# Optimization experiments

Hardware: AMD Instinct MI355X
Metric: run time of the kernel (lower is better)

## Reference

```python
import jax, jax.numpy as jnp
import numpy as np

N = 100000   # nodes
E = 1000000  # directed edges
IN = 32      # atom feature dim
H = 64       # hidden_channels
ED = 16      # edge_dim
OUT = 1      # out_channels
G = 512      # graphs in batch
SLOPE = 0.2  # GATConv leaky_relu negative_slope


def setup_inputs() -> dict:
    key = jax.random.key(0)
    ks = jax.random.split(key, 20)
    s = 0.1
    return {
        'x': jax.random.normal(ks[0], (N, IN), dtype=jnp.float32),
        'edge_attr': jax.random.normal(ks[1], (E, ED), dtype=jnp.float32),
        'w_node': jax.random.normal(ks[2], (IN, H), dtype=jnp.float32) * s,
        'b_node': jnp.zeros((H,), jnp.float32),
        'w_edge': jax.random.normal(ks[3], (ED, H), dtype=jnp.float32) * s,
        'b_edge': jnp.zeros((H,), jnp.float32),
        'conv_W': jax.random.normal(ks[4], (3, H, H), dtype=jnp.float32) * s,
        'conv_We': jax.random.normal(ks[5], (3, H, H), dtype=jnp.float32) * s,
        'conv_att_s': jax.random.normal(ks[6], (3, H), dtype=jnp.float32) * s,
        'conv_att_d': jax.random.normal(ks[7], (3, H), dtype=jnp.float32) * s,
        'conv_att_e': jax.random.normal(ks[8], (3, H), dtype=jnp.float32) * s,
        'conv_b': jnp.zeros((3, H), jnp.float32),
        'gru_Wih': jax.random.normal(ks[9], (3, H, 3 * H), dtype=jnp.float32) * s,
        'gru_Whh': jax.random.normal(ks[10], (3, H, 3 * H), dtype=jnp.float32) * s,
        'gru_bih': jnp.zeros((3, 3 * H), jnp.float32),
        'gru_bhh': jnp.zeros((3, 3 * H), jnp.float32),
        'w_out': jax.random.normal(ks[11], (H, OUT), dtype=jnp.float32) * s,
        'b_out': jnp.zeros((OUT,), jnp.float32),
        'edge_index': jax.random.randint(ks[12], (2, E), 0, N),
        'batch': jnp.sort(jax.random.randint(ks[13], (N,), 0, G)),
    }


def _gat_layer(x, e, src, dst, W, att_s, att_d, att_e, b):
    # PyG GATConv (heads=1, concat=False): shared lin for src/dst,
    # edge features enter only the attention score.
    h = x @ W                                   # [N, H]
    a = jax.nn.leaky_relu(h[src] @ att_s + h[dst] @ att_d + e @ att_e, SLOPE)
    m = jax.lax.stop_gradient(jax.ops.segment_max(a, dst, num_segments=N))
    m = jnp.where(jnp.isfinite(m), m, 0.0)
    ex = jnp.exp(a - m[dst])
    den = jax.ops.segment_sum(ex, dst, num_segments=N)
    alpha = ex / den[dst]                       # segment softmax per destination
    out = jax.ops.segment_sum(alpha[:, None] * h[src], dst, num_segments=N)
    return out + b


def _gru_cell(inp, hid, Wih, Whh, bih, bhh):
    gi = inp @ Wih + bih
    gh = hid @ Whh + bhh
    ir, iz, inn = jnp.split(gi, 3, axis=-1)
    hr, hz, hn = jnp.split(gh, 3, axis=-1)
    r = jax.nn.sigmoid(ir + hr)
    z = jax.nn.sigmoid(iz + hz)
    n = jnp.tanh(inn + r * hn)
    return (1.0 - z) * n + z * hid


def reference(x, edge_attr, w_node, b_node, w_edge, b_edge, conv_W, conv_We,
              conv_att_s, conv_att_d, conv_att_e, conv_b, gru_Wih, gru_Whh,
              gru_bih, gru_bhh, w_out, b_out, edge_index, batch):
    src, dst = edge_index[0], edge_index[1]
    xi = jax.nn.relu(x @ w_node + b_node)             # [N, H]
    ea = jax.nn.relu(edge_attr @ w_edge + b_edge)     # [E, H]
    # PyG add_self_loops(fill_value='mean'): self-loop edge_attr = mean of
    # incoming edge_attr per destination node (0 if no in-edges).
    cnt = jax.ops.segment_sum(jnp.ones((E,), xi.dtype), dst, num_segments=N)
    esum = jax.ops.segment_sum(ea, dst, num_segments=N)
    ea_loop = jnp.where(cnt[:, None] > 0, esum / jnp.maximum(cnt, 1.0)[:, None], 0.0)
    loops = jnp.arange(N)
    src2 = jnp.concatenate([src, loops])
    dst2 = jnp.concatenate([dst, loops])
    ea2 = jnp.concatenate([ea, ea_loop], axis=0)      # [E+N, H]
    for i in range(3):
        e = ea2 @ conv_We[i]
        h = jax.nn.relu(_gat_layer(xi, e, src2, dst2, conv_W[i],
                                   conv_att_s[i], conv_att_d[i],
                                   conv_att_e[i], conv_b[i]))
        # dropout p=0.0 is identity
        xi = jax.nn.relu(_gru_cell(h, xi, gru_Wih[i], gru_Whh[i],
                                   gru_bih[i], gru_bhh[i]))
    pooled = jax.ops.segment_sum(xi, batch, num_segments=G)  # global_add_pool
    return pooled @ w_out + b_out                            # [G, 1]
```

## Files before the change

### kernel.cpp

```cpp
#include <hip/hip_runtime.h>
#include <hip/hip_fp16.h>

constexpr int H_  = 64;
constexpr int DIN = 32;
constexpr int DE  = 16;
constexpr int BNODE = 512;
constexpr int ACH   = 2048;
constexpr int CAP   = 6144;
#define SLOPE 0.2f

typedef __attribute__((ext_vector_type(8))) short bf16x8;
typedef __attribute__((ext_vector_type(4))) float f32x4;

__device__ __forceinline__ float sigm_(float x){ return 1.0f/(1.0f+__expf(-x)); }
__device__ __forceinline__ float tanh_(float x){ float e=__expf(2.0f*x); return 1.0f - 2.0f/(e+1.0f); }
__device__ __forceinline__ short f2bf(float f){
  unsigned u = __float_as_uint(f);
  u += 0x7FFF + ((u>>16)&1);
  return (short)(u>>16);
}
__device__ __forceinline__ float bf2f(unsigned short s){
  return __uint_as_float(((unsigned)s)<<16);
}
__device__ __forceinline__ float h2f_(unsigned hb){
  return __half2float(__ushort_as_half((unsigned short)hb));
}

__global__ void k_prep(const float* __restrict__ w_node, const float* __restrict__ w_edge,
                       const float* __restrict__ conv_W, const float* __restrict__ gWih,
                       const float* __restrict__ gWhh, const float* __restrict__ conv_We,
                       const float* __restrict__ att_e,
                       short* __restrict__ wnT16, short* __restrict__ weT16p,
                       short* __restrict__ cWT16, short* __restrict__ WihT16,
                       short* __restrict__ WhhT16, float* __restrict__ ve,
                       int* __restrict__ bcur){
  int id = blockIdx.x*blockDim.x + threadIdx.x;
  if (id < 2048){
    int j = id >> 5, k = id & 31;
    wnT16[id] = f2bf(w_node[k*64 + j]);
    return;
  }
  id -= 2048;
  if (id < 2048){
    int j = id >> 5, k = id & 31;
    weT16p[id] = (k < DE) ? f2bf(w_edge[k*64 + j]) : (short)0;
    return;
  }
  id -= 2048;
  if (id < 12288){
    int l = id / 4096, rem = id & 4095, j = rem >> 6, k = rem & 63;
    cWT16[id] = f2bf(conv_W[l*4096 + k*64 + j]);
    return;
  }
  id -= 12288;
  if (id < 36864){
    int l = id / 12288, rem = id % 12288, j = rem >> 6, k = rem & 63;
    WihT16[id] = f2bf(gWih[l*12288 + k*192 + j]);
    return;
  }
  id -= 36864;
  if (id < 36864){
    int l = id / 12288, rem = id % 12288, j = rem >> 6, k = rem & 63;
    WhhT16[id] = f2bf(gWhh[l*12288 + k*192 + j]);
    return;
  }
  id -= 36864;
  if (id < 192){
    int l = id >> 6, k = id & 63;
    const float* w = conv_We + (size_t)(l*64+k)*64;
    const float* a = att_e + l*64;
    float s = 0.f;
    #pragma unroll
    for (int j=0;j<64;j++) s += w[j]*a[j];
    ve[id] = s;
    return;
  }
  id -= 192;
  if (id < 256) bcur[id] = id*CAP;
}

__global__ void __launch_bounds__(256,4)
k_nmlp_m(const float* __restrict__ x, const short* __restrict__ wT16,
         const float* __restrict__ b, short* __restrict__ xi, int N){
  int lane = threadIdx.x & 63, w = threadIdx.x >> 6;
  int m16 = lane & 15, kb = lane >> 4;
  int n0 = blockIdx.x*64 + w*16;
  int arow = n0 + m16; if (arow > N-1) arow = N-1;
  const float* xr = x + (size_t)arow*DIN + kb*8;
  float4 a0 = *(const float4*)xr, a1 = *(const float4*)(xr+4);
  bf16x8 af;
  af[0]=f2bf(a0.x); af[1]=f2bf(a0.y); af[2]=f2bf(a0.z); af[3]=f2bf(a0.w);
  af[4]=f2bf(a1.x); af[5]=f2bf(a1.y); af[6]=f2bf(a1.z); af[7]=f2bf(a1.w);
  f32x4 acc[4];
  #pragma unroll
  for (int t=0;t<4;t++) acc[t]=(f32x4){0.f,0.f,0.f,0.f};
  const short* wp = wT16 + (size_t)m16*DIN + kb*8;
  #pragma unroll
  for (int t=0;t<4;t++){
    bf16x8 bb = *(const bf16x8*)(wp + (size_t)(t*16)*DIN);
    acc[t] = __builtin_amdgcn_mfma_f32_16x16x32_bf16(af, bb, acc[t], 0,0,0);
  }
  int mrow = (lane>>4)*4;
  #pragma unroll
  for (int t=0;t<4;t++){
    int f = t*16 + m16;
    float bj = b[f];
    #pragma unroll
    for (int q=0;q<4;q++){
      int node = n0 + mrow + q;
      if (node < N) xi[(size_t)node*H_ + f] = f2bf(fmaxf(acc[t][q] + bj, 0.f));
    }
  }
}

__global__ void __launch_bounds__(256,4)
k_edge_m(const float* __restrict__ attr, const short* __restrict__ weT16p,
         const float* __restrict__ be, const float* __restrict__ ve,
         const int* __restrict__ src, uint2* __restrict__ esc8, int E){
  int lane = threadIdx.x & 63, w = threadIdx.x >> 6;
  int m16 = lane & 15, kb = lane >> 4;
  int e0 = (blockIdx.x*4 + w)*16;
  if (e0 >= E) return;
  bf16x8 af = {0,0,0,0,0,0,0,0};
  if (kb < 2){
    int arow = e0 + m16; if (arow > E-1) arow = E-1;
    const float* ap = attr + (size_t)arow*DE + kb*8;
    float4 a0 = *(const float4*)ap, a1 = *(const float4*)(ap+4);
    af[0]=f2bf(a0.x); af[1]=f2bf(a0.y); af[2]=f2bf(a0.z); af[3]=f2bf(a0.w);
    af[4]=f2bf(a1.x); af[5]=f2bf(a1.y); af[6]=f2bf(a1.z); af[7]=f2bf(a1.w);
  }
  f32x4 acc[4];
  #pragma unroll
  for (int t=0;t<4;t++) acc[t]=(f32x4){0.f,0.f,0.f,0.f};
  const short* wp = weT16p + (size_t)m16*32 + kb*8;
  #pragma unroll
  for (int t=0;t<4;t++){
    bf16x8 bb = *(const bf16x8*)(wp + (size_t)(t*16)*32);
    acc[t] = __builtin_amdgcn_mfma_f32_16x16x32_bf16(af, bb, acc[t], 0,0,0);
  }
  int mrow = (lane>>4)*4;
  float s0[4]={0.f,0.f,0.f,0.f}, s1[4]={0.f,0.f,0.f,0.f}, s2[4]={0.f,0.f,0.f,0.f};
  #pragma unroll
  for (int t=0;t<4;t++){
    int j = t*16 + m16;
    float bj = be[j];
    float v0 = ve[j], v1 = ve[64+j], v2 = ve[128+j];
    #pragma unroll
    for (int q=0;q<4;q++){
      float ea = fmaxf(acc[t][q] + bj, 0.f);
      s0[q] = fmaf(ea, v0, s0[q]);
      s1[q] = fmaf(ea, v1, s1[q]);
      s2[q] = fmaf(ea, v2, s2[q]);
    }
  }
  #pragma unroll
  for (int d=1; d<16; d<<=1){
    #pragma unroll
    for (int q=0;q<4;q++){
      s0[q] += __shfl_xor(s0[q], d);
      s1[q] += __shfl_xor(s1[q], d);
      s2[q] += __shfl_xor(s2[q], d);
    }
  }
  if (m16==0){
    #pragma unroll
    for (int q=0;q<4;q++){
      int e = e0 + mrow + q;
      if (e < E){
        unsigned sv = (unsigned)src[e];
        unsigned h0 = (__half_as_ushort(__float2half(s0[q])) & 0xFFFEu) | (sv >> 16);
        unsigned h1 = __half_as_ushort(__float2half(s1[q]));
        unsigned h2 = __half_as_ushort(__float2half(s2[q]));
        esc8[e] = make_uint2(h0 | (h1<<16), (sv & 0xFFFFu) | (h2<<16));
      }
    }
  }
}

__global__ void __launch_bounds__(256)
k_binA(const uint2* __restrict__ esc8, const int* __restrict__ dst,
       int* __restrict__ bcur, uint2* __restrict__ bin8, unsigned short* __restrict__ bin2,
       int E){
  __shared__ int cnt[256];
  __shared__ int ofs[256];
  __shared__ int gofs[256];
  __shared__ uint2 st8[ACH];
  __shared__ unsigned short st2[ACH];
  __shared__ unsigned char sbid[ACH];
  int tid = threadIdx.x;
  int base = blockIdx.x * ACH;
  cnt[tid] = 0;
  __syncthreads();
  uint2 r8[8]; int bb[8]; int ms[8]; int dl[8];
  #pragma unroll
  for (int k=0;k<8;k++){
    int e = base + tid + k*256;
    bb[k] = -1;
    if (e < E){
      r8[k] = esc8[e];
      int d = dst[e];
      bb[k] = d >> 9;
      dl[k] = d & (BNODE-1);
      ms[k] = atomicAdd(&cnt[bb[k]], 1);
    }
  }
  __syncthreads();
  int v = cnt[tid];
  ofs[tid] = v;
  __syncthreads();
  for (int d=1; d<256; d<<=1){
    int t = 0;
    if (tid>=d) t = ofs[tid-d];
    __syncthreads();
    if (tid>=d) ofs[tid] += t;
    __syncthreads();
  }
  int total = ofs[255];
  int excl = ofs[tid] - v;
  __syncthreads();
  ofs[tid] = excl;
  __syncthreads();
  #pragma unroll
  for (int k=0;k<8;k++){
    if (bb[k] >= 0){
      int slot = ofs[bb[k]] + ms[k];
      st8[slot] = r8[k];
      st2[slot] = (unsigned short)dl[k];
      sbid[slot] = (unsigned char)bb[k];
    }
  }
  if (v > 0) gofs[tid] = atomicAdd(&bcur[tid], v);
  __syncthreads();
  for (int slot = tid; slot < total; slot += 256){
    int b = sbid[slot];
    int gp = gofs[b] + (slot - ofs[b]);
    bin8[gp] = st8[slot];
    bin2[gp] = st2[slot];
  }
}

__global__ void __launch_bounds__(256)
k_hist(const unsigned short* __restrict__ bin2, const int* __restrict__ bcur,
       int* __restrict__ deg, int N){
  __shared__ int lcnt[BNODE];
  int b = blockIdx.x;
  int n0 = b*BNODE;
  int n1 = n0 + BNODE; if (n1 > N) n1 = N;
  int nn = n1 - n0;
  for (int i = threadIdx.x; i < nn; i += 256) lcnt[i] = 0;
  __syncthreads();
  int beg = b*CAP, cntb = bcur[b] - beg;
  for (int idx = threadIdx.x; idx < cntb; idx += 256)
    atomicAdd(&lcnt[bin2[beg+idx]], 1);
  __syncthreads();
  for (int i = threadIdx.x; i < nn; i += 256) deg[n0+i] = lcnt[i] + 1;
}

__global__ void k_bsum(const int* __restrict__ deg, int* __restrict__ bsum, int N){
  int i = blockIdx.x*256 + threadIdx.x;
  int v = (i<N) ? deg[i] : 0;
  #pragma unroll
  for(int d=32; d; d>>=1) v += __shfl_xor(v, d);
  __shared__ int sh[4];
  if ((threadIdx.x&63)==0) sh[threadIdx.x>>6] = v;
  __syncthreads();
  if (threadIdx.x==0) bsum[blockIdx.x] = sh[0]+sh[1]+sh[2]+sh[3];
}

__global__ void k_bscan(const int* __restrict__ bsum, int* __restrict__ boff, int NB,
                        int* __restrict__ offN, int EN){
  __shared__ int sh[1024];
  int tid = threadIdx.x;
  int v = (tid<NB) ? bsum[tid] : 0;
  sh[tid] = v;
  __syncthreads();
  for(int d=1; d<1024; d<<=1){
    int t = 0;
    if (tid>=d) t = sh[tid-d];
    __syncthreads();
    if (tid>=d) sh[tid] += t;
    __syncthreads();
  }
  if (tid<NB) boff[tid] = sh[tid] - v;
  if (tid==0) offN[0] = EN;
}

__global__ void k_scan_fin(const int* __restrict__ deg, const int* __restrict__ boff,
                           int* __restrict__ off, int N){
  __shared__ int sh[256];
  int i = blockIdx.x*256 + threadIdx.x;
  int v = (i<N) ? deg[i] : 0;
  sh[threadIdx.x] = v;
  __syncthreads();
  for(int d=1; d<256; d<<=1){
    int t = 0;
    if (threadIdx.x>=d) t = sh[threadIdx.x-d];
    __syncthreads();
    if (threadIdx.x>=d) sh[threadIdx.x] += t;
    __syncthreads();
  }
  if (i<N) off[i] = boff[blockIdx.x] + sh[threadIdx.x] - v;
}

__global__ void __launch_bounds__(256)
k_binB(const uint2* __restrict__ bin8, const unsigned short* __restrict__ bin2,
       const int* __restrict__ bcur, const int* __restrict__ off,
       uint2* __restrict__ rec, int N){
  __shared__ int lcur[BNODE];
  int b = blockIdx.x;
  int n0 = b*BNODE;
  int n1 = n0 + BNODE; if (n1 > N) n1 = N;
  int nn = n1 - n0;
  for (int i = threadIdx.x; i < nn; i += 256) lcur[i] = off[n0+i] + 1;
  __syncthreads();
  int beg = b*CAP, cntb = bcur[b] - beg;
  for (int idx = threadIdx.x; idx < cntb; idx += 256){
    uint2 r = bin8[beg+idx];
    int dl = bin2[beg+idx];
    int p = atomicAdd(&lcur[dl], 1);
    rec[p] = r;
  }
}

__global__ void k_selfloop_csr(const int* __restrict__ off, uint2* __restrict__ rec, int N){
  int n = blockIdx.x*blockDim.x+threadIdx.x;
  if (n>=N) return;
  int a = off[n]+1, b = off[n+1];
  float s0=0.f,s1=0.f,s2=0.f;
  for (int p=a;p<b;p++){
    uint2 r=rec[p];
    s0 += h2f_(r.x & 0xFFFEu);
    s1 += h2f_(r.x >> 16);
    s2 += h2f_(r.y >> 16);
  }
  float inv = (b>a) ? 1.0f/(float)(b-a) : 0.0f;
  unsigned h0 = __half_as_ushort(__float2half(s0*inv)) & 0xFFFEu;
  unsigned h1 = __half_as_ushort(__float2half(s1*inv));
  unsigned h2 = __half_as_ushort(__float2half(s2*inv));
  unsigned s = (unsigned)n;
  rec[off[n]] = make_uint2(h0 | (s>>16) | (h1<<16), (s & 0xFFFFu) | (h2<<16));
}

__global__ void k_gbounds(const int* __restrict__ batch, int* __restrict__ gstart, int N, int G){
  int n = blockIdx.x*blockDim.x+threadIdx.x;
  if (n>=N) return;
  int b = batch[n];
  int bp = (n==0) ? -1 : batch[n-1];
  for (int g=bp+1; g<=b; g++) gstart[g]=n;
  if (n==N-1){ for (int g=b+1; g<=G; g++) gstart[g]=N; }
}

__global__ void __launch_bounds__(256,2)
k_gru_m(const short* __restrict__ hg16, const short* __restrict__ xin, short* __restrict__ xout,
        const short* __restrict__ WihT16, const short* __restrict__ WhhT16,
        const float* __restrict__ bih, const float* __restrict__ bhh, int N){
  int lane = threadIdx.x & 63, w = threadIdx.x >> 6;
  int m16 = lane & 15;
  int kb  = lane >> 4;
  int n0 = blockIdx.x*128 + w*32;

  int r0 = n0 + m16;      if (r0 > N-1) r0 = N-1;
  int r1 = n0 + 16 + m16; if (r1 > N-1) r1 = N-1;
  const short* h0p = hg16 + (size_t)r0*H_ + kb*8;
  const short* h1p = hg16 + (size_t)r1*H_ + kb*8;
  bf16x8 ah0a = *(const bf16x8*)(h0p), ah1a = *(const bf16x8*)(h0p+32);
  bf16x8 ah0b = *(const bf16x8*)(h1p), ah1b = *(const bf16x8*)(h1p+32);
  const short* x0p = xin + (size_t)r0*H_ + kb*8;
  const short* x1p = xin + (size_t)r1*H_ + kb*8;
  bf16x8 ax0a = *(const bf16x8*)(x0p), ax1a = *(const bf16x8*)(x0p+32);
  bf16x8 ax0b = *(const bf16x8*)(x1p), ax1b = *(const bf16x8*)(x1p+32);

  f32x4 aR[2][4], aZ[2][4], aNi[2][4], aNh[2][4];
  #pragma unroll
  for (int s=0;s<2;s++){
    #pragma unroll
    for (int t=0;t<4;t++){
      aR[s][t]=(f32x4){0.f,0.f,0.f,0.f}; aZ[s][t]=(f32x4){0.f,0.f,0.f,0.f};
      aNi[s][t]=(f32x4){0.f,0.f,0.f,0.f}; aNh[s][t]=(f32x4){0.f,0.f,0.f,0.f};
    }
  }

  const short* wi = WihT16 + (size_t)m16*H_ + kb*8;
  const short* wh = WhhT16 + (size_t)m16*H_ + kb*8;
  #pragma unroll
  for (int t=0;t<4;t++){
    bf16x8 b;
    b = *(const bf16x8*)(wi + (size_t)(t*16)*H_);
    aR[0][t] = __builtin_amdgcn_mfma_f32_16x16x32_bf16(ah0a, b, aR[0][t], 0,0,0);
    aR[1][t] = __builtin_amdgcn_mfma_f32_16x16x32_bf16(ah0b, b, aR[1][t], 0,0,0);
    b = *(const bf16x8*)(wi + (size_t)(t*16)*H_ + 32);
    aR[0][t] = __builtin_amdgcn_mfma_f32_16x16x32_bf16(ah1a, b, aR[0][t], 0,0,0);
    aR[1][t] = __builtin_amdgcn_mfma_f32_16x16x32_bf16(ah1b, b, aR[1][t], 0,0,0);
    b = *(const bf16x8*)(wh + (size_t)(t*16)*H_);
    aR[0][t] = __builtin_amdgcn_mfma_f32_16x16x32_bf16(ax0a, b, aR[0][t], 0,0,0);
    aR[1][t] = __builtin_amdgcn_mfma_f32_16x16x32_bf16(ax0b, b, aR[1][t], 0,0,0);
    b = *(const bf16x8*)(wh + (size_t)(t*16)*H_ + 32);
    aR[0][t] = __builtin_amdgcn_mfma_f32_16x16x32_bf16(ax1a, b, aR[0][t], 0,0,0);
    aR[1][t] = __builtin_amdgcn_mfma_f32_16x16x32_bf16(ax1b, b, aR[1][t], 0,0,0);

    b = *(const bf16x8*)(wi + (size_t)(64+t*16)*H_);
    aZ[0][t] = __builtin_amdgcn_mfma_f32_16x16x32_bf16(ah0a, b, aZ[0][t], 0,0,0);
    aZ[1][t] = __builtin_amdgcn_mfma_f32_16x16x32_bf16(ah0b, b, aZ[1][t], 0,0,0);
    b = *(const bf16x8*)(wi + (size_t)(64+t*16)*H_ + 32);
    aZ[0][t] = __builtin_amdgcn_mfma_f32_16x16x32_bf16(ah1a, b, aZ[0][t], 0,0,0);
    aZ[1][t] = __builtin_amdgcn_mfma_f32_16x16x32_bf16(ah1b, b, aZ[1][t], 0,0,0);
    b = *(const bf16x8*)(wh + (size_t)(64+t*16)*H_);
    aZ[0][t] = __builtin_amdgcn_mfma_f32_16x16x32_bf16(ax0a, b, aZ[0][t], 0,0,0);
    aZ[1][t] = __builtin_amdgcn_mfma_f32_16x16x32_bf16(ax0b, b, aZ[1][t], 0,0,0);
    b = *(const bf16x8*)(wh + (size_t)(64+t*16)*H_ + 32);
    aZ[0][t] = __builtin_amdgcn_mfma_f32_16x16x32_bf16(ax1a, b, aZ[0][t], 0,0,0);
    aZ[1][t] = __builtin_amdgcn_mfma_f32_16x16x32_bf16(ax1b, b, aZ[1][t], 0,0,0);

    b = *(const bf16x8*)(wi + (size_t)(128+t*16)*H_);
    aNi[0][t] = __builtin_amdgcn_mfma_f32_16x16x32_bf16(ah0a, b, aNi[0][t], 0,0,0);
    aNi[1][t] = __builtin_amdgcn_mfma_f32_16x16x32_bf16(ah0b, b, aNi[1][t], 0,0,0);
    b = *(const bf16x8*)(wi + (size_t)(128+t*16)*H_ + 32);
    aNi[0][t] = __builtin_amdgcn_mfma_f32_16x16x32_bf16(ah1a, b, aNi[0][t], 0,0,0);
    aNi[1][t] = __builtin_amdgcn_mfma_f32_16x16x32_bf16(ah1b, b, aNi[1][t], 0,0,0);
    b = *(const bf16x8*)(wh + (size_t)(128+t*16)*H_);
    aNh[0][t] = __builtin_amdgcn_mfma_f32_16x16x32_bf16(ax0a, b, aNh[0][t], 0,0,0);
    aNh[1][t] = __builtin_amdgcn_mfma_f32_16x16x32_bf16(ax0b, b, aNh[1][t], 0,0,0);
    b = *(const bf16x8*)(wh + (size_t)(128+t*16)*H_ + 32);
    aNh[0][t] = __builtin_amdgcn_mfma_f32_16x16x32_bf16(ax1a, b, aNh[0][t], 0,0,0);
    aNh[1][t] = __builtin_amdgcn_mfma_f32_16x16x32_bf16(ax1b, b, aNh[1][t], 0,0,0);
  }

  int mrow = (lane>>4)*4;
  #pragma unroll
  for (int s=0;s<2;s++){
    #pragma unroll
    for (int t=0;t<4;t++){
      int f = t*16 + m16;
      float br = bih[f]     + bhh[f];
      float bz = bih[64+f]  + bhh[64+f];
      float bin= bih[128+f], bhn = bhh[128+f];
      #pragma unroll
      for (int q=0;q<4;q++){
        int node = n0 + s*16 + mrow + q;
        if (node < N){
          float r  = sigm_(aR[s][t][q] + br);
          float z  = sigm_(aZ[s][t][q] + bz);
          float nn = tanh_(aNi[s][t][q] + bin + r*(aNh[s][t][q] + bhn));
          float xv = bf2f((unsigned short)xin[(size_t)node*H_ + f]);
          xout[(size_t)node*H_ + f] = f2bf(fmaxf((1.f-z)*nn + z*xv, 0.f));
        }
      }
    }
  }
}

__global__ void __launch_bounds__(256,4)
k_linh_m(const short* __restrict__ xi, const short* __restrict__ wT16,
         const float* __restrict__ atts, const float* __restrict__ attd,
         __half* __restrict__ h16, float* __restrict__ ssc, float* __restrict__ dsc, int N){
  int lane = threadIdx.x & 63, w = threadIdx.x >> 6;
  int m16 = lane & 15, kb = lane >> 4;
  int n0 = blockIdx.x*128 + w*32;
  int r0 = n0 + m16;      if (r0 > N-1) r0 = N-1;
  int r1 = n0 + 16 + m16; if (r1 > N-1) r1 = N-1;
  const short* x0p = xi + (size_t)r0*H_ + kb*8;
  const short* x1p = xi + (size_t)r1*H_ + kb*8;
  bf16x8 ax0a = *(const bf16x8*)(x0p), ax1a = *(const bf16x8*)(x0p+32);
  bf16x8 ax0b = *(const bf16x8*)(x1p), ax1b = *(const bf16x8*)(x1p+32);

  f32x4 acc[2][4];
  #pragma unroll
  for (int s=0;s<2;s++)
    #pragma unroll
    for (int t=0;t<4;t++) acc[s][t]=(f32x4){0.f,0.f,0.f,0.f};
  const short* wp = wT16 + (size_t)m16*H_ + kb*8;
  #pragma unroll
  for (int t=0;t<4;t++){
    bf16x8 b0 = *(const bf16x8*)(wp + (size_t)(t*16)*H_);
    acc[0][t] = __builtin_amdgcn_mfma_f32_16x16x32_bf16(ax0a, b0, acc[0][t], 0,0,0);
    acc[1][t] = __builtin_amdgcn_mfma_f32_16x16x32_bf16(ax0b, b0, acc[1][t], 0,0,0);
    bf16x8 b1 = *(const bf16x8*)(wp + (size_t)(t*16)*H_ + 32);
    acc[0][t] = __builtin_amdgcn_mfma_f32_16x16x32_bf16(ax1a, b1, acc[0][t], 0,0,0);
    acc[1][t] = __builtin_amdgcn_mfma_f32_16x16x32_bf16(ax1b, b1, acc[1][t], 0,0,0);
  }

  int mrow = (lane>>4)*4;
  float ps[2][4], pd[2][4];
  #pragma unroll
  for (int s=0;s<2;s++)
    #pragma unroll
    for (int q=0;q<4;q++){ ps[s][q]=0.f; pd[s][q]=0.f; }
  #pragma unroll
  for (int t=0;t<4;t++){
    int f = t*16 + m16;
    float as = atts[f], ad = attd[f];
    #pragma unroll
    for (int s=0;s<2;s++){
      #pragma unroll
      for (int q=0;q<4;q++){
        int node = n0 + s*16 + mrow + q;
        float v = acc[s][t][q];
        if (node < N) h16[(size_t)node*H_ + f] = __float2half(v);
        ps[s][q] = fmaf(v, as, ps[s][q]); pd[s][q] = fmaf(v, ad, pd[s][q]);
      }
    }
  }
  #pragma unroll
  for (int d=1; d<16; d<<=1){
    #pragma unroll
    for (int s=0;s<2;s++)
      #pragma unroll
      for (int q=0;q<4;q++){ ps[s][q] += __shfl_xor(ps[s][q], d); pd[s][q] += __shfl_xor(pd[s][q], d); }
  }
  if (m16==0){
    #pragma unroll
    for (int s=0;s<2;s++){
      #pragma unroll
      for (int q=0;q<4;q++){
        int node = n0 + s*16 + mrow + q;
        if (node < N){ ssc[node]=ps[s][q]; dsc[node]=pd[s][q]; }
      }
    }
  }
}

template<int L>
__global__ void __launch_bounds__(256)
k_gat_g4(const __half* __restrict__ h16, const float* __restrict__ ssc,
         const float* __restrict__ dsc, const uint2* __restrict__ rec,
         const int* __restrict__ off, const float* __restrict__ bias,
         short* __restrict__ hgat16, int N){
  int lane = threadIdx.x & 63, w = threadIdx.x >> 6;
  int g = lane >> 4, fl = lane & 15;
  int node = blockIdx.x*16 + w*4 + g;
  if (node >= N) return;
  int e0 = off[node], e1 = off[node+1];
  float dval = dsc[node];
  float acc0=0.f, acc1=0.f, acc2=0.f, acc3=0.f, den=0.f;
  int gbase = lane & 48;
  for (int base = e0; base < e1; base += 16){
    int p = base + fl;
    float ex = 0.f; int s = 0;
    if (p < e1){
      uint2 r = rec[p];
      s = (int)((r.y & 0xFFFFu) | ((r.x & 1u) << 16));
      unsigned hb = (L==0) ? (r.x & 0xFFFEu) : (L==1) ? (r.x >> 16) : (r.y >> 16);
      float a = ssc[s] + dval + h2f_(hb);
      a = (a > 0.f) ? a : SLOPE*a;
      ex = __expf(a);
    }
    den += ex;
    int cnt = e1 - base; if (cnt > 16) cnt = 16;
    for (int j = 0; j < cnt; j++){
      float exb = __shfl(ex, gbase + j);
      int   sb  = __shfl(s,  gbase + j);
      uint2 hv = *(const uint2*)(h16 + (size_t)sb*H_ + 4*fl);
      float2 f0 = __half22float2(*(__half2*)&hv.x);
      float2 f1 = __half22float2(*(__half2*)&hv.y);
      acc0 = fmaf(exb, f0.x, acc0);
      acc1 = fmaf(exb, f0.y, acc1);
      acc2 = fmaf(exb, f1.x, acc2);
      acc3 = fmaf(exb, f1.y, acc3);
    }
  }
  #pragma unroll
  for (int d=1; d<16; d<<=1) den += __shfl_xor(den, d);
  float4 bv = *(const float4*)(bias + 4*fl);
  float inv = 1.0f/den;
  float v0 = fmaxf(fmaf(acc0,inv,bv.x), 0.f);
  float v1 = fmaxf(fmaf(acc1,inv,bv.y), 0.f);
  float v2 = fmaxf(fmaf(acc2,inv,bv.z), 0.f);
  float v3 = fmaxf(fmaf(acc3,inv,bv.w), 0.f);
  uint2 o;
  o.x = ((unsigned)(unsigned short)f2bf(v1)<<16) | (unsigned short)f2bf(v0);
  o.y = ((unsigned)(unsigned short)f2bf(v3)<<16) | (unsigned short)f2bf(v2);
  *(uint2*)(hgat16 + (size_t)node*H_ + 4*fl) = o;
}

__global__ void __launch_bounds__(256)
k_pool_g(const short* __restrict__ xi, const float* __restrict__ wout,
         const int* __restrict__ gstart, const float* __restrict__ b_out,
         float* __restrict__ out){
  int g = blockIdx.x;
  int a = gstart[g], b = gstart[g+1];
  float acc = 0.f;
  for (int n = a + threadIdx.x; n < b; n += 256){
    const uint4* xr = (const uint4*)(xi + (size_t)n*H_);
    float s = 0.f;
    #pragma unroll
    for (int q=0;q<8;q++){
      uint4 v = xr[q];
      s += bf2f((unsigned short)(v.x&0xFFFF))*wout[8*q]   + bf2f((unsigned short)(v.x>>16))*wout[8*q+1]
         + bf2f((unsigned short)(v.y&0xFFFF))*wout[8*q+2] + bf2f((unsigned short)(v.y>>16))*wout[8*q+3]
         + bf2f((unsigned short)(v.z&0xFFFF))*wout[8*q+4] + bf2f((unsigned short)(v.z>>16))*wout[8*q+5]
         + bf2f((unsigned short)(v.w&0xFFFF))*wout[8*q+6] + bf2f((unsigned short)(v.w>>16))*wout[8*q+7];
    }
    acc += s;
  }
  #pragma unroll
  for (int d=32; d; d>>=1) acc += __shfl_xor(acc, d);
  __shared__ float sh[4];
  if ((threadIdx.x&63)==0) sh[threadIdx.x>>6] = acc;
  __syncthreads();
  if (threadIdx.x==0) out[g] = sh[0]+sh[1]+sh[2]+sh[3] + b_out[0];
}

extern "C" void kernel_launch(void* const* d_in, const int* in_sizes, int n_in,
                              void* d_out, int out_size, void* d_ws, size_t ws_size,
                              hipStream_t stream){
  const float* x       = (const float*)d_in[0];
  const float* eattr   = (const float*)d_in[1];
  const float* w_node  = (const float*)d_in[2];
  const float* b_node  = (const float*)d_in[3];
  const float* w_edge  = (const float*)d_in[4];
  const float* b_edge  = (const float*)d_in[5];
  const float* conv_W  = (const float*)d_in[6];
  const float* conv_We = (const float*)d_in[7];
  const float* att_s   = (const float*)d_in[8];
  const float* att_d   = (const float*)d_in[9];
  const float* att_e   = (const float*)d_in[10];
  const float* conv_b  = (const float*)d_in[11];
  const float* gWih    = (const float*)d_in[12];
  const float* gWhh    = (const float*)d_in[13];
  const float* gbih    = (const float*)d_in[14];
  const float* gbhh    = (const float*)d_in[15];
  const float* w_out   = (const float*)d_in[16];
  const float* b_out   = (const float*)d_in[17];
  const int*   eidx    = (const int*)d_in[18];
  const int*   batch   = (const int*)d_in[19];
  float* out = (float*)d_out;

  int N = in_sizes[0]/DIN;
  int E = in_sizes[1]/DE;
  int G = out_size;
  int EN = E + N;
  const int* src = eidx;
  const int* dst = eidx + E;

  char* p = (char*)d_ws;
  auto carve = [&](size_t bytes)->void*{ void* r=(void*)p; p += (bytes+255)&~(size_t)255; return r; };
  short*  xi0    = (short*)carve((size_t)N*H_*2);
  short*  xi1    = (short*)carve((size_t)N*H_*2);
  __half* h16    = (__half*)carve((size_t)N*H_*2);
  short*  hgat16 = (short*)carve((size_t)N*H_*2);
  float*  ssc    = (float*)carve((size_t)N*4);
  float*  dsc    = (float*)carve((size_t)N*4);
  uint2*  esc8   = (uint2*)carve((size_t)E*8);
  uint2*  rec    = (uint2*)carve((size_t)EN*8);
  uint2*  bin8   = (uint2*)carve((size_t)256*CAP*8);
  unsigned short* bin2 = (unsigned short*)carve((size_t)256*CAP*2);
  int*    deg    = (int*)carve((size_t)N*4);
  int*    off    = (int*)carve((size_t)(N+1)*4);
  int*    bcur   = (int*)carve((size_t)256*4);
  int*    gstart = (int*)carve((size_t)(G+1)*4);
  int*    bsum   = (int*)carve((size_t)1024*4);
  int*    boff   = (int*)carve((size_t)1024*4);
  short*  wnT16  = (short*)carve((size_t)DIN*H_*2);
  short*  weT16p = (short*)carve((size_t)64*32*2);
  short*  cWT16  = (short*)carve((size_t)3*H_*H_*2);
  short*  WihT16 = (short*)carve((size_t)3*192*H_*2);
  short*  WhhT16 = (short*)carve((size_t)3*192*H_*2);
  float*  ve     = (float*)carve((size_t)3*H_*4);

  auto cdiv=[](int a,int b){return (a+b-1)/b;};
  int NB  = cdiv(N,256);
  int NBK = cdiv(N,BNODE);

  int prep_total = 2048+2048+12288+36864+36864+192+256;
  k_prep<<<cdiv(prep_total,256),256,0,stream>>>(w_node, w_edge, conv_W, gWih, gWhh, conv_We, att_e,
                                                wnT16, weT16p, cWT16, WihT16, WhhT16, ve, bcur);
  k_nmlp_m<<<cdiv(N,64),256,0,stream>>>(x, wnT16, b_node, xi0, N);
  k_edge_m<<<cdiv(E,64),256,0,stream>>>(eattr, weT16p, b_edge, ve, src, esc8, E);
  k_binA<<<cdiv(E,ACH),256,0,stream>>>(esc8, dst, bcur, bin8, bin2, E);
  k_hist<<<NBK,256,0,stream>>>(bin2, bcur, deg, N);
  k_bsum<<<NB,256,0,stream>>>(deg, bsum, N);
  k_bscan<<<1,1024,0,stream>>>(bsum, boff, NB, off+N, EN);
  k_scan_fin<<<NB,256,0,stream>>>(deg, boff, off, N);
  k_binB<<<NBK,256,0,stream>>>(bin8, bin2, bcur, off, rec, N);
  k_selfloop_csr<<<cdiv(N,256),256,0,stream>>>(off, rec, N);
  k_gbounds<<<NB,256,0,stream>>>(batch, gstart, N, G);

  int NB128 = cdiv(N,128);
  int NB16  = cdiv(N,16);
  for (int l=0; l<3; l++){
    const short* xin = (l&1) ? xi1 : xi0;
    short*       xo  = (l&1) ? xi0 : xi1;
    k_linh_m<<<NB128,256,0,stream>>>(xin, cWT16 + (size_t)l*H_*H_, att_s + l*H_, att_d + l*H_,
                                     h16, ssc, dsc, N);
    if (l==0)      k_gat_g4<0><<<NB16,256,0,stream>>>(h16, ssc, dsc, rec, off, conv_b + l*H_, hgat16, N);
    else if (l==1) k_gat_g4<1><<<NB16,256,0,stream>>>(h16, ssc, dsc, rec, off, conv_b + l*H_, hgat16, N);
    else           k_gat_g4<2><<<NB16,256,0,stream>>>(h16, ssc, dsc, rec, off, conv_b + l*H_, hgat16, N);
    k_gru_m<<<NB128,256,0,stream>>>(hgat16, xin, xo, WihT16 + (size_t)l*192*H_, WhhT16 + (size_t)l*192*H_,
                                    gbih + l*3*H_, gbhh + l*3*H_, N);
  }

  k_pool_g<<<G,256,0,stream>>>(xi1, w_out, gstart, b_out, out);
}
```

Baseline: 378.4 us.

## Fuse CSR build, self-loop mean and graph bounds into fewer kernels

Replaces the global histogram, three-pass prefix scan, scatter and self-loop kernels with one per-bucket kernel. It counts, scans locally and scatters into a padded per-bucket CSR region with separate start and end offsets, and it accumulates the self-loop means in shared memory with atomics. Graph-boundary computation moves into the prep kernel, and the edge bias is folded into the MFMA through a constant-one input column. This removes several launches and global passes, at the cost of a larger padded rec buffer, shared-memory float atomics, and a different floating-point summation order for the self-loop means.

```diff
diff --git a/kernel.cpp b/kernel.cpp
--- a/kernel.cpp
+++ b/kernel.cpp
@@ -7,6 +7,7 @@
 constexpr int BNODE = 512;
 constexpr int ACH   = 2048;
 constexpr int CAP   = 6144;
+constexpr int CAP2  = CAP + BNODE;
 #define SLOPE 0.2f
 
 typedef __attribute__((ext_vector_type(8))) short bf16x8;
@@ -27,13 +28,14 @@
 }
 
 __global__ void k_prep(const float* __restrict__ w_node, const float* __restrict__ w_edge,
+                       const float* __restrict__ b_edge,
                        const float* __restrict__ conv_W, const float* __restrict__ gWih,
                        const float* __restrict__ gWhh, const float* __restrict__ conv_We,
-                       const float* __restrict__ att_e,
+                       const float* __restrict__ att_e, const int* __restrict__ batch,
                        short* __restrict__ wnT16, short* __restrict__ weT16p,
                        short* __restrict__ cWT16, short* __restrict__ WihT16,
                        short* __restrict__ WhhT16, float* __restrict__ ve,
-                       int* __restrict__ bcur){
+                       int* __restrict__ bcur, int* __restrict__ gstart, int N, int G){
   int id = blockIdx.x*blockDim.x + threadIdx.x;
   if (id < 2048){
     int j = id >> 5, k = id & 31;
@@ -43,7 +45,7 @@
   id -= 2048;
   if (id < 2048){
     int j = id >> 5, k = id & 31;
-    weT16p[id] = (k < DE) ? f2bf(w_edge[k*64 + j]) : (short)0;
+    weT16p[id] = (k < DE) ? f2bf(w_edge[k*64 + j]) : (k == DE ? f2bf(b_edge[j]) : (short)0);
     return;
   }
   id -= 2048;
@@ -76,7 +78,14 @@
     return;
   }
   id -= 192;
-  if (id < 256) bcur[id] = id*CAP;
+  if (id < 256){ bcur[id] = id*CAP; return; }
+  id -= 256;
+  if (id < N){
+    int b = batch[id];
+    int bp = (id==0) ? -1 : batch[id-1];
+    for (int g=bp+1; g<=b; g++) gstart[g]=id;
+    if (id==N-1){ for (int g=b+1; g<=G; g++) gstart[g]=N; }
+  }
 }
 
 __global__ void __launch_bounds__(256,4)
@@ -115,8 +124,8 @@
 
 __global__ void __launch_bounds__(256,4)
 k_edge_m(const float* __restrict__ attr, const short* __restrict__ weT16p,
-         const float* __restrict__ be, const float* __restrict__ ve,
-         const int* __restrict__ src, uint2* __restrict__ esc8, int E){
+         const float* __restrict__ ve, const int* __restrict__ src,
+         uint2* __restrict__ esc8, int E){
   int lane = threadIdx.x & 63, w = threadIdx.x >> 6;
   int m16 = lane & 15, kb = lane >> 4;
   int e0 = (blockIdx.x*4 + w)*16;
@@ -128,6 +137,8 @@
     float4 a0 = *(const float4*)ap, a1 = *(const float4*)(ap+4);
     af[0]=f2bf(a0.x); af[1]=f2bf(a0.y); af[2]=f2bf(a0.z); af[3]=f2bf(a0.w);
     af[4]=f2bf(a1.x); af[5]=f2bf(a1.y); af[6]=f2bf(a1.z); af[7]=f2bf(a1.w);
+  } else if (kb == 2){
+    af[0] = (short)0x3F80;
   }
   f32x4 acc[4];
   #pragma unroll
@@ -143,11 +154,10 @@
   #pragma unroll
   for (int t=0;t<4;t++){
     int j = t*16 + m16;
-    float bj = be[j];
     float v0 = ve[j], v1 = ve[64+j], v2 = ve[128+j];
     #pragma unroll
     for (int q=0;q<4;q++){
-      float ea = fmaxf(acc[t][q] + bj, 0.f);
+      float ea = fmaxf(acc[t][q], 0.f);
       s0[q] = fmaf(ea, v0, s0[q]);
       s1[q] = fmaf(ea, v1, s1[q]);
       s2[q] = fmaf(ea, v2, s2[q]);
@@ -240,114 +250,59 @@
 }
 
 __global__ void __launch_bounds__(256)
-k_hist(const unsigned short* __restrict__ bin2, const int* __restrict__ bcur,
-       int* __restrict__ deg, int N){
+k_binB2(const uint2* __restrict__ bin8, const unsigned short* __restrict__ bin2,
+        const int* __restrict__ bcur, int* __restrict__ offS, int* __restrict__ offE,
+        uint2* __restrict__ rec, int N){
   __shared__ int lcnt[BNODE];
-  int b = blockIdx.x;
+  __shared__ int lcur[BNODE];
+  __shared__ int loffS[BNODE];
+  __shared__ int sc[256];
+  __shared__ float ls0[BNODE], ls1[BNODE], ls2[BNODE];
+  int b = blockIdx.x, tid = threadIdx.x;
   int n0 = b*BNODE;
   int n1 = n0 + BNODE; if (n1 > N) n1 = N;
   int nn = n1 - n0;
-  for (int i = threadIdx.x; i < nn; i += 256) lcnt[i] = 0;
+  for (int i=tid;i<BNODE;i+=256){ lcnt[i]=0; ls0[i]=0.f; ls1[i]=0.f; ls2[i]=0.f; }
   __syncthreads();
   int beg = b*CAP, cntb = bcur[b] - beg;
-  for (int idx = threadIdx.x; idx < cntb; idx += 256)
-    atomicAdd(&lcnt[bin2[beg+idx]], 1);
-  __syncthreads();
-  for (int i = threadIdx.x; i < nn; i += 256) deg[n0+i] = lcnt[i] + 1;
-}
-
-__global__ void k_bsum(const int* __restrict__ deg, int* __restrict__ bsum, int N){
-  int i = blockIdx.x*256 + threadIdx.x;
-  int v = (i<N) ? deg[i] : 0;
-  #pragma unroll
-  for(int d=32; d; d>>=1) v += __shfl_xor(v, d);
-  __shared__ int sh[4];
-  if ((threadIdx.x&63)==0) sh[threadIdx.x>>6] = v;
-  __syncthreads();
-  if (threadIdx.x==0) bsum[blockIdx.x] = sh[0]+sh[1]+sh[2]+sh[3];
-}
-
-__global__ void k_bscan(const int* __restrict__ bsum, int* __restrict__ boff, int NB,
-                        int* __restrict__ offN, int EN){
-  __shared__ int sh[1024];
-  int tid = threadIdx.x;
-  int v = (tid<NB) ? bsum[tid] : 0;
-  sh[tid] = v;
-  __syncthreads();
-  for(int d=1; d<1024; d<<=1){
-    int t = 0;
-    if (tid>=d) t = sh[tid-d];
+  for (int idx=tid; idx<cntb; idx+=256) atomicAdd(&lcnt[bin2[beg+idx]], 1);
+  __syncthreads();
+  int i0 = 2*tid, i1 = 2*tid+1;
+  int a0 = (i0<nn) ? lcnt[i0]+1 : 0;
+  int a1 = (i1<nn) ? lcnt[i1]+1 : 0;
+  int pair = a0+a1;
+  sc[tid] = pair;
+  __syncthreads();
+  for (int d=1; d<256; d<<=1){
+    int t = 0; if (tid>=d) t = sc[tid-d];
     __syncthreads();
-    if (tid>=d) sh[tid] += t;
+    if (tid>=d) sc[tid] += t;
     __syncthreads();
   }
-  if (tid<NB) boff[tid] = sh[tid] - v;
-  if (tid==0) offN[0] = EN;
-}
-
-__global__ void k_scan_fin(const int* __restrict__ deg, const int* __restrict__ boff,
-                           int* __restrict__ off, int N){
-  __shared__ int sh[256];
-  int i = blockIdx.x*256 + threadIdx.x;
-  int v = (i<N) ? deg[i] : 0;
-  sh[threadIdx.x] = v;
-  __syncthreads();
-  for(int d=1; d<256; d<<=1){
-    int t = 0;
-    if (threadIdx.x>=d) t = sh[threadIdx.x-d];
-    __syncthreads();
-    if (threadIdx.x>=d) sh[threadIdx.x] += t;
-    __syncthreads();
-  }
-  if (i<N) off[i] = boff[blockIdx.x] + sh[threadIdx.x] - v;
-}
-
-__global__ void __launch_bounds__(256)
-k_binB(const uint2* __restrict__ bin8, const unsigned short* __restrict__ bin2,
-       const int* __restrict__ bcur, const int* __restrict__ off,
-       uint2* __restrict__ rec, int N){
-  __shared__ int lcur[BNODE];
-  int b = blockIdx.x;
-  int n0 = b*BNODE;
-  int n1 = n0 + BNODE; if (n1 > N) n1 = N;
-  int nn = n1 - n0;
-  for (int i = threadIdx.x; i < nn; i += 256) lcur[i] = off[n0+i] + 1;
-  __syncthreads();
-  int beg = b*CAP, cntb = bcur[b] - beg;
-  for (int idx = threadIdx.x; idx < cntb; idx += 256){
+  int excl = sc[tid] - pair;
+  int base = b*CAP2;
+  if (i0<nn){ int o=base+excl;    offS[n0+i0]=o; offE[n0+i0]=o+a0; loffS[i0]=o; lcur[i0]=o+1; }
+  if (i1<nn){ int o=base+excl+a0; offS[n0+i1]=o; offE[n0+i1]=o+a1; loffS[i1]=o; lcur[i1]=o+1; }
+  __syncthreads();
+  for (int idx=tid; idx<cntb; idx+=256){
     uint2 r = bin8[beg+idx];
     int dl = bin2[beg+idx];
     int p = atomicAdd(&lcur[dl], 1);
     rec[p] = r;
-  }
-}
-
-__global__ void k_selfloop_csr(const int* __restrict__ off, uint2* __restrict__ rec, int N){
-  int n = blockIdx.x*blockDim.x+threadIdx.x;
-  if (n>=N) return;
-  int a = off[n]+1, b = off[n+1];
-  float s0=0.f,s1=0.f,s2=0.f;
-  for (int p=a;p<b;p++){
-    uint2 r=rec[p];
-    s0 += h2f_(r.x & 0xFFFEu);
-    s1 += h2f_(r.x >> 16);
-    s2 += h2f_(r.y >> 16);
-  }
-  float inv = (b>a) ? 1.0f/(float)(b-a) : 0.0f;
-  unsigned h0 = __half_as_ushort(__float2half(s0*inv)) & 0xFFFEu;
-  unsigned h1 = __half_as_ushort(__float2half(s1*inv));
-  unsigned h2 = __half_as_ushort(__float2half(s2*inv));
-  unsigned s = (unsigned)n;
-  rec[off[n]] = make_uint2(h0 | (s>>16) | (h1<<16), (s & 0xFFFFu) | (h2<<16));
-}
-
-__global__ void k_gbounds(const int* __restrict__ batch, int* __restrict__ gstart, int N, int G){
-  int n = blockIdx.x*blockDim.x+threadIdx.x;
-  if (n>=N) return;
-  int b = batch[n];
-  int bp = (n==0) ? -1 : batch[n-1];
-  for (int g=bp+1; g<=b; g++) gstart[g]=n;
-  if (n==N-1){ for (int g=b+1; g<=G; g++) gstart[g]=N; }
+    atomicAdd(&ls0[dl], h2f_(r.x & 0xFFFEu));
+    atomicAdd(&ls1[dl], h2f_(r.x >> 16));
+    atomicAdd(&ls2[dl], h2f_(r.y >> 16));
+  }
+  __syncthreads();
+  for (int i=tid; i<nn; i+=256){
+    int cnt = lcnt[i];
+    float inv = (cnt>0) ? 1.0f/(float)cnt : 0.0f;
+    unsigned h0 = __half_as_ushort(__float2half(ls0[i]*inv)) & 0xFFFEu;
+    unsigned h1 = __half_as_ushort(__float2half(ls1[i]*inv));
+    unsigned h2 = __half_as_ushort(__float2half(ls2[i]*inv));
+    unsigned s = (unsigned)(n0+i);
+    rec[loffS[i]] = make_uint2(h0 | (s>>16) | (h1<<16), (s & 0xFFFFu) | (h2<<16));
+  }
 }
 
 __global__ void __launch_bounds__(256,2)
@@ -523,13 +478,13 @@
 __global__ void __launch_bounds__(256)
 k_gat_g4(const __half* __restrict__ h16, const float* __restrict__ ssc,
          const float* __restrict__ dsc, const uint2* __restrict__ rec,
-         const int* __restrict__ off, const float* __restrict__ bias,
-         short* __restrict__ hgat16, int N){
+         const int* __restrict__ offS, const int* __restrict__ offE,
+         const float* __restrict__ bias, short* __restrict__ hgat16, int N){
   int lane = threadIdx.x & 63, w = threadIdx.x >> 6;
   int g = lane >> 4, fl = lane & 15;
   int node = blockIdx.x*16 + w*4 + g;
   if (node >= N) return;
-  int e0 = off[node], e1 = off[node+1];
+  int e0 = offS[node], e1 = offE[node];
   float dval = dsc[node];
   float acc0=0.f, acc1=0.f, acc2=0.f, acc3=0.f, den=0.f;
   int gbase = lane & 48;
@@ -628,7 +583,6 @@
   int N = in_sizes[0]/DIN;
   int E = in_sizes[1]/DE;
   int G = out_size;
-  int EN = E + N;
   const int* src = eidx;
   const int* dst = eidx + E;
 
@@ -641,15 +595,13 @@
   float*  ssc    = (float*)carve((size_t)N*4);
   float*  dsc    = (float*)carve((size_t)N*4);
   uint2*  esc8   = (uint2*)carve((size_t)E*8);
-  uint2*  rec    = (uint2*)carve((size_t)EN*8);
+  uint2*  rec    = (uint2*)carve((size_t)256*CAP2*8);
   uint2*  bin8   = (uint2*)carve((size_t)256*CAP*8);
   unsigned short* bin2 = (unsigned short*)carve((size_t)256*CAP*2);
-  int*    deg    = (int*)carve((size_t)N*4);
-  int*    off    = (int*)carve((size_t)(N+1)*4);
+  int*    offS   = (int*)carve((size_t)N*4);
+  int*    offE   = (int*)carve((size_t)N*4);
   int*    bcur   = (int*)carve((size_t)256*4);
   int*    gstart = (int*)carve((size_t)(G+1)*4);
-  int*    bsum   = (int*)carve((size_t)1024*4);
-  int*    boff   = (int*)carve((size_t)1024*4);
   short*  wnT16  = (short*)carve((size_t)DIN*H_*2);
   short*  weT16p = (short*)carve((size_t)64*32*2);
   short*  cWT16  = (short*)carve((size_t)3*H_*H_*2);
@@ -658,22 +610,17 @@
   float*  ve     = (float*)carve((size_t)3*H_*4);
 
   auto cdiv=[](int a,int b){return (a+b-1)/b;};
-  int NB  = cdiv(N,256);
   int NBK = cdiv(N,BNODE);
 
-  int prep_total = 2048+2048+12288+36864+36864+192+256;
-  k_prep<<<cdiv(prep_total,256),256,0,stream>>>(w_node, w_edge, conv_W, gWih, gWhh, conv_We, att_e,
-                                                wnT16, weT16p, cWT16, WihT16, WhhT16, ve, bcur);
+  int prep_total = 2048+2048+12288+36864+36864+192+256+N;
+  k_prep<<<cdiv(prep_total,256),256,0,stream>>>(w_node, w_edge, b_edge, conv_W, gWih, gWhh,
+                                                conv_We, att_e, batch,
+                                                wnT16, weT16p, cWT16, WihT16, WhhT16, ve,
+                                                bcur, gstart, N, G);
   k_nmlp_m<<<cdiv(N,64),256,0,stream>>>(x, wnT16, b_node, xi0, N);
-  k_edge_m<<<cdiv(E,64),256,0,stream>>>(eattr, weT16p, b_edge, ve, src, esc8, E);
+  k_edge_m<<<cdiv(E,64),256,0,stream>>>(eattr, weT16p, ve, src, esc8, E);
   k_binA<<<cdiv(E,ACH),256,0,stream>>>(esc8, dst, bcur, bin8, bin2, E);
-  k_hist<<<NBK,256,0,stream>>>(bin2, bcur, deg, N);
-  k_bsum<<<NB,256,0,stream>>>(deg, bsum, N);
-  k_bscan<<<1,1024,0,stream>>>(bsum, boff, NB, off+N, EN);
-  k_scan_fin<<<NB,256,0,stream>>>(deg, boff, off, N);
-  k_binB<<<NBK,256,0,stream>>>(bin8, bin2, bcur, off, rec, N);
-  k_selfloop_csr<<<cdiv(N,256),256,0,stream>>>(off, rec, N);
-  k_gbounds<<<NB,256,0,stream>>>(batch, gstart, N, G);
+  k_binB2<<<NBK,256,0,stream>>>(bin8, bin2, bcur, offS, offE, rec, N);
 
   int NB128 = cdiv(N,128);
   int NB16  = cdiv(N,16);
@@ -682,9 +629,9 @@
     short*       xo  = (l&1) ? xi0 : xi1;
     k_linh_m<<<NB128,256,0,stream>>>(xin, cWT16 + (size_t)l*H_*H_, att_s + l*H_, att_d + l*H_,
                                      h16, ssc, dsc, N);
-    if (l==0)      k_gat_g4<0><<<NB16,256,0,stream>>>(h16, ssc, dsc, rec, off, conv_b + l*H_, hgat16, N);
-    else if (l==1) k_gat_g4<1><<<NB16,256,0,stream>>>(h16, ssc, dsc, rec, off, conv_b + l*H_, hgat16, N);
-    else           k_gat_g4<2><<<NB16,256,0,stream>>>(h16, ssc, dsc, rec, off, conv_b + l*H_, hgat16, N);
+    if (l==0)      k_gat_g4<0><<<NB16,256,0,stream>>>(h16, ssc, dsc, rec, offS, offE, conv_b + l*H_, hgat16, N);
+    else if (l==1) k_gat_g4<1><<<NB16,256,0,stream>>>(h16, ssc, dsc, rec, offS, offE, conv_b + l*H_, hgat16, N);
+    else           k_gat_g4<2><<<NB16,256,0,stream>>>(h16, ssc, dsc, rec, offS, offE, conv_b + l*H_, hgat16, N);
     k_gru_m<<<NB128,256,0,stream>>>(hgat16, xin, xo, WihT16 + (size_t)l*192*H_, WhhT16 + (size_t)l*192*H_,
                                     gbih + l*3*H_, gbhh + l*3*H_, N);
   }
```

Result: no change. 374.3 us (-1.1%).
